# Optimization experiments

Hardware: AMD Instinct MI355X
Metric: run time of the kernel (lower is better)

Reference implementation:

```python
import jax, jax.numpy as jnp
import numpy as np

N = 25000      # nodes
E = 300000     # edges
IN = 32        # in_dim
EDF = 16       # edge_feat_dim
HID = 256      # hidden_dim (per-head dim, concat=False)
HEADS = 4
ACT = 16       # num_actions
G = 64         # graphs in batch
KW = 1024      # wire-mask query nodes


def setup_inputs() -> dict:
    key = jax.random.key(0)
    ks = jax.random.split(key, 20)
    def rn(k, shape, s=0.1):
        return jax.random.normal(k, shape, jnp.float32) * s
    return {
        "x": jax.random.normal(ks[0], (N, IN), jnp.float32),
        "edge_attr": jax.random.normal(ks[1], (E, EDF), jnp.float32),
        "wire_mask": jax.random.randint(ks[2], (KW,), 0, N, jnp.int32),
        "edge_index": jax.random.randint(ks[3], (2, E), 0, N, jnp.int32),
        "batch": jnp.sort(jax.random.randint(ks[4], (N,), 0, G, jnp.int32)),
        "enc_w1": rn(ks[5], (EDF, 32)),
        "enc_b1": jnp.zeros((32,), jnp.float32),
        "enc_w2": rn(ks[6], (32, IN * IN), 0.05),
        "enc_b2": jnp.zeros((IN * IN,), jnp.float32),
        "root_w": rn(ks[7], (IN, IN)),
        "nn_bias": jnp.zeros((IN,), jnp.float32),
        "gat1_w": rn(ks[8], (IN, HEADS * HID)),
        "gat1_asrc": rn(ks[9], (HEADS, HID)),
        "gat1_adst": rn(ks[10], (HEADS, HID)),
        "gat1_b": jnp.zeros((HID,), jnp.float32),
        "gat2_w": rn(ks[11], (HID, HEADS * HID)),
        "gat2_asrc": rn(ks[12], (HEADS, HID)),
        "gat2_adst": rn(ks[13], (HEADS, HID)),
        "gat2_b": jnp.zeros((HID,), jnp.float32),
        "wire_w": rn(ks[14], (HID, 1)),
        "wire_b": jnp.zeros((1,), jnp.float32),
        "act_w": rn(ks[15], (HID, ACT)),
        "act_b": jnp.zeros((ACT,), jnp.float32),
    }


def _gat(x, src, dst, W, a_src, a_dst, b):
    # PyG GATConv, concat=False (mean over heads), eval mode (no dropout),
    # self-loops already included in (src, dst).
    H, D = a_src.shape
    h = (x @ W).reshape(-1, H, D)                      # [N, H, D]
    es = (h * a_src[None]).sum(-1)                     # [N, H]
    ed = (h * a_dst[None]).sum(-1)                     # [N, H]
    e = jax.nn.leaky_relu(es[src] + ed[dst], negative_slope=0.2)  # [E2, H]
    m = jax.ops.segment_max(e, dst, num_segments=N)    # segment softmax (stable)
    w = jnp.exp(e - m[dst])
    den = jax.ops.segment_sum(w, dst, num_segments=N)
    alpha = w / (den[dst] + 1e-16)
    out = jax.ops.segment_sum(h[src] * alpha[..., None], dst, num_segments=N)
    return out.mean(axis=1) + b                        # [N, D]


def reference(x, edge_attr, wire_mask, edge_index, batch,
              enc_w1, enc_b1, enc_w2, enc_b2, root_w, nn_bias,
              gat1_w, gat1_asrc, gat1_adst, gat1_b,
              gat2_w, gat2_asrc, gat2_adst, gat2_b,
              wire_w, wire_b, act_w, act_b):
    src, dst = edge_index[0], edge_index[1]
    # NNConv (aggr='mean'): per-edge weight matrix from edge MLP
    We = (jax.nn.relu(edge_attr @ enc_w1 + enc_b1) @ enc_w2 + enc_b2)
    We = We.reshape(E, IN, IN)                         # [E, in, out]
    msg = jnp.einsum('ei,eio->eo', x[src], We)         # [E, out]
    s = jax.ops.segment_sum(msg, dst, num_segments=N)
    cnt = jax.ops.segment_sum(jnp.ones((E,), x.dtype), dst, num_segments=N)
    agg = s / jnp.maximum(cnt, 1.0)[:, None]
    h0 = jax.nn.relu(agg + x @ root_w + nn_bias)
    # GATConv default add_self_loops=True
    sl = jnp.arange(N, dtype=src.dtype)
    src2 = jnp.concatenate([src, sl])
    dst2 = jnp.concatenate([dst, sl])
    h1 = jax.nn.relu(_gat(h0, src2, dst2, gat1_w, gat1_asrc, gat1_adst, gat1_b))
    h2 = jax.nn.relu(_gat(h1, src2, dst2, gat2_w, gat2_asrc, gat2_adst, gat2_b))
    p_wire = (h2[wire_mask] @ wire_w + wire_b).squeeze(-1)   # [KW]
    pooled_s = jax.ops.segment_sum(h2, batch, num_segments=G)
    gc = jax.ops.segment_sum(jnp.ones((N,), h2.dtype), batch, num_segments=G)
    pooled = pooled_s / jnp.maximum(gc, 1.0)[:, None]        # global_mean_pool
    p_action = pooled @ act_w + act_b                        # [G, ACT]
    return (p_wire, p_action)
```

## Files before the change

kernel.cpp:

```cpp
#include <hip/hip_runtime.h>
#include <hip/hip_fp16.h>

#define N_NODES 25000
#define M_PAD   25024
#define N_TILES 1564
#define N_EDGES 300000
#define IN_DIM  32
#define EDFD    16
#define HIDD    256
#define HEADS   4
#define NACT    16
#define NGRAPH  64
#define KWIRE   1024
#define POOL_NB 64

typedef _Float16 half8v __attribute__((ext_vector_type(8)));
typedef __attribute__((ext_vector_type(4))) float f32x4;

__device__ __forceinline__ float leaky(float v) { return v > 0.f ? v : 0.2f * v; }

__global__ __launch_bounds__(256) void k_deg2(const int* __restrict__ ei,
                                              int* __restrict__ deg,
                                              int* __restrict__ deg2) {
    int e = blockIdx.x * 256 + threadIdx.x;
    if (e >= N_EDGES) return;
    atomicAdd(&deg[ei[N_EDGES + e]], 1);
    atomicAdd(&deg2[ei[e]], 1);
}

__global__ __launch_bounds__(256) void k_scan2(const int* __restrict__ degA, int* __restrict__ rpA,
                                               const int* __restrict__ degB, int* __restrict__ rpB) {
    const int* deg = blockIdx.x ? degB : degA;
    int* rowptr    = blockIdx.x ? rpB : rpA;
    __shared__ int part[256];
    int t = threadIdx.x;
    const int CH = 98;
    int base = t * CH;
    int s = 0;
    for (int i = 0; i < CH; ++i) {
        int idx = base + i;
        if (idx < N_NODES) s += deg[idx];
    }
    part[t] = s;
    __syncthreads();
    if (t == 0) {
        int run = 0;
        for (int i = 0; i < 256; ++i) { int v = part[i]; part[i] = run; run += v; }
    }
    __syncthreads();
    int run = part[t];
    for (int i = 0; i < CH; ++i) {
        int idx = base + i;
        if (idx < N_NODES) { rowptr[idx] = run; run += deg[idx]; }
    }
    if (N_NODES >= base && N_NODES < base + CH) rowptr[N_NODES] = run;
}

__global__ __launch_bounds__(256) void k_scatter2(const int* __restrict__ ei,
                                                  const float* __restrict__ ea,
                                                  const int* __restrict__ rowptr,
                                                  const int* __restrict__ rowptr2,
                                                  int* __restrict__ cursor,
                                                  int* __restrict__ cursor2,
                                                  int* __restrict__ csrc,
                                                  int* __restrict__ cdst,
                                                  int* __restrict__ posMap,
                                                  __half* __restrict__ eaP) {
    int e = blockIdx.x * 256 + threadIdx.x;
    if (e >= N_EDGES) return;
    int src = ei[e], dst = ei[N_EDGES + e];
    int p1 = atomicAdd(&cursor[dst], 1);
    int r1 = rowptr[dst] + p1;
    csrc[r1] = src;
    int p2 = atomicAdd(&cursor2[src], 1);
    int r2 = rowptr2[src] + p2;
    cdst[r2] = dst;
    posMap[r2] = r1;
    const float4* src4 = (const float4*)(ea + (size_t)e * EDFD);
    __half2* dp = (__half2*)(eaP + (size_t)r2 * EDFD);
    #pragma unroll
    for (int q = 0; q < EDFD / 4; ++q) {
        float4 v = src4[q];
        dp[q * 2]     = __float22half2_rn(make_float2(v.x, v.y));
        dp[q * 2 + 1] = __float22half2_rn(make_float2(v.z, v.w));
    }
}

__global__ __launch_bounds__(256) void k_prep(const float* __restrict__ w2,
                                              const float* __restrict__ W1,
                                              const float* __restrict__ W2,
                                              const float* __restrict__ a1s,
                                              const float* __restrict__ a1d,
                                              const float* __restrict__ a2s,
                                              const float* __restrict__ a2d,
                                              const float* __restrict__ x,
                                              const float* __restrict__ b2,
                                              const float* __restrict__ w1,
                                              __half* __restrict__ wtt,
                                              __half* __restrict__ wb1,
                                              __half* __restrict__ wb2,
                                              float* __restrict__ wa1,
                                              float* __restrict__ wd1,
                                              float* __restrict__ wa2,
                                              float* __restrict__ wd2,
                                              __half* __restrict__ xf,
                                              float* __restrict__ xb,
                                              __half* __restrict__ w1t) {
    int bid = blockIdx.x, t = threadIdx.x;
    if (bid < 128) {
        int idx = bid * 256 + t;
        int co = idx >> 5, i = idx & 31;
        wtt[idx] = __float2half(w2[(co >> 5) * 1024 + i * 32 + (co & 31)]);
    } else if (bid < 256) {
        int idx = (bid - 128) * 256 + t;
        int d = idx >> 7, k = idx & 127;
        int h = k >> 5, i = k & 31;
        wb1[idx] = __float2half(0.25f * W1[i * 1024 + h * 256 + d]);
    } else if (bid < 1280) {
        int idx = (bid - 256) * 256 + t;
        int d = idx >> 10, k = idx & 1023;
        int h = k >> 8, i = k & 255;
        wb2[idx] = __float2half(0.25f * W2[i * 1024 + h * 256 + d]);
    } else if (bid < 4405) {
        int idx = (bid - 1280) * 256 + t;
        if (idx >= N_NODES * 32) return;
        int n = idx >> 5, o = idx & 31;
        xf[idx] = __float2half(x[idx]);
        float s = 0.f;
        for (int i = 0; i < 32; ++i) s += x[n * 32 + i] * b2[i * 32 + o];
        xb[idx] = s;
    } else if (bid == 4405) {
        if (t >= 128) return;
        int h = t >> 5, i = t & 31;
        float s = 0.f, sd = 0.f;
        for (int d = 0; d < 256; ++d) {
            float w = W1[i * 1024 + h * 256 + d];
            s  += w * a1s[h * 256 + d];
            sd += w * a1d[h * 256 + d];
        }
        wa1[t] = s; wd1[t] = sd;
    } else if (bid < 4410) {
        int idx = (bid - 4406) * 256 + t;
        if (idx >= 1024) return;
        int h = idx >> 8, i = idx & 255;
        float s = 0.f, sd = 0.f;
        for (int d = 0; d < 256; ++d) {
            float w = W2[i * 1024 + h * 256 + d];
            s  += w * a2s[h * 256 + d];
            sd += w * a2d[h * 256 + d];
        }
        wa2[idx] = s; wd2[idx] = sd;
    } else {
        int idx = (bid - 4410) * 256 + t;
        if (idx >= 32 * EDFD) return;
        int j = idx >> 4, k = idx & 15;
        w1t[idx] = __float2half(w1[k * 32 + j]);
    }
}

__global__ __launch_bounds__(256) void k_msg3(const int* __restrict__ rowptr2,
                                              const int* __restrict__ posMap,
                                              const __half* __restrict__ eaP,
                                              const __half* __restrict__ w1t,
                                              const float* __restrict__ b1,
                                              const __half* __restrict__ T,
                                              const float* __restrict__ xb,
                                              __half* __restrict__ msgE) {
    int wv = threadIdx.x >> 6, lane = threadIdx.x & 63;
    int src = blockIdx.x * 4 + wv;
    if (src >= N_NODES) return;
    int r0 = rowptr2[src], r1 = rowptr2[src + 1];
    if (r0 == r1) return;
    int lr = lane & 15, lk = (lane >> 4) * 8;

    half8v bf0, bf1;
    const __half* Tp = T + (size_t)src * 1024;
    #pragma unroll
    for (int q = 0; q < 8; ++q) {
        bf0[q] = (_Float16)__half2float(Tp[(lk + q) * 32 + lr]);
        bf1[q] = (_Float16)__half2float(Tp[(lk + q) * 32 + 16 + lr]);
    }

    __half2 w1r[8][EDFD / 2];
    #pragma unroll
    for (int q = 0; q < 8; ++q) {
        const __half2* wp = (const __half2*)(w1t + (lk + q) * EDFD);
        #pragma unroll
        for (int k2 = 0; k2 < EDFD / 2; ++k2) w1r[q][k2] = wp[k2];
    }
    float b1r[8];
    #pragma unroll
    for (int q = 0; q < 8; ++q) b1r[q] = b1[lk + q];

    float xb0 = xb[src * 32 + lr], xb1 = xb[src * 32 + 16 + lr];
    int rbase = (lane >> 4) * 4;

    for (int t0 = r0; t0 < r1; t0 += 16) {
        int e = t0 + lr;
        bool ok = (e < r1);
        half8v afr;
        if (ok) {
            const __half2* ep = (const __half2*)(eaP + (size_t)e * EDFD);
            __half2 ea2[EDFD / 2];
            #pragma unroll
            for (int k2 = 0; k2 < EDFD / 2; ++k2) ea2[k2] = ep[k2];
            #pragma unroll
            for (int q = 0; q < 8; ++q) {
                float s = b1r[q];
                #pragma unroll
                for (int k2 = 0; k2 < EDFD / 2; ++k2) {
                    float2 v = __half22float2(ea2[k2]);
                    float2 w = __half22float2(w1r[q][k2]);
                    s += v.x * w.x + v.y * w.y;
                }
                afr[q] = (_Float16)fmaxf(s, 0.f);
            }
        } else {
            #pragma unroll
            for (int q = 0; q < 8; ++q) afr[q] = (_Float16)0.f;
        }
        f32x4 c0 = {0.f, 0.f, 0.f, 0.f}, c1 = {0.f, 0.f, 0.f, 0.f};
        c0 = __builtin_amdgcn_mfma_f32_16x16x32_f16(afr, bf0, c0, 0, 0, 0);
        c1 = __builtin_amdgcn_mfma_f32_16x16x32_f16(afr, bf1, c1, 0, 0, 0);
        #pragma unroll
        for (int r = 0; r < 4; ++r) {
            int er = t0 + rbase + r;
            if (er < r1) {
                int pm = posMap[er];
                msgE[(size_t)pm * 32 + lr]      = __float2half(c0[r] + xb0);
                msgE[(size_t)pm * 32 + 16 + lr] = __float2half(c1[r] + xb1);
            }
        }
    }
}

__global__ __launch_bounds__(256) void k_h0e(const float* __restrict__ x,
                                             const float* __restrict__ root_w,
                                             const float* __restrict__ nn_bias,
                                             const __half* __restrict__ msgE,
                                             const int* __restrict__ rowptr,
                                             const float* __restrict__ wa,
                                             const float* __restrict__ wd,
                                             __half* __restrict__ h0f,
                                             float* __restrict__ es,
                                             float* __restrict__ ed) {
    int t = threadIdx.x;
    int ng = t >> 5, o = t & 31;
    int n = blockIdx.x * 8 + ng;
    if (n >= N_NODES) return;
    float s = nn_bias[o];
    for (int k = 0; k < IN_DIM; ++k) s += x[n * IN_DIM + k] * root_w[k * 32 + o];
    int r0 = rowptr[n], r1 = rowptr[n + 1];
    float aggv = 0.f;
    for (int r = r0; r < r1; ++r)
        aggv += __half2float(msgE[(size_t)r * 32 + o]);
    float c = fmaxf((float)(r1 - r0), 1.f);
    s += aggv / c;
    float v = fmaxf(s, 0.f);
    h0f[n * IN_DIM + o] = __float2half(v);
    #pragma unroll
    for (int h = 0; h < 4; ++h) {
        float ss = v * wa[h * 32 + o];
        float dd = v * wd[h * 32 + o];
        #pragma unroll
        for (int off = 16; off; off >>= 1) {
            ss += __shfl_down(ss, off, 32);
            dd += __shfl_down(dd, off, 32);
        }
        if (o == 0) { es[n * 4 + h] = ss; ed[n * 4 + h] = dd; }
    }
}

__global__ __launch_bounds__(256, 2) void k_gemT(const __half* __restrict__ A,
                                                 const __half* __restrict__ Wt,
                                                 __half* __restrict__ C) {
    __shared__ __half cst[4][16 * 36];
    int t = threadIdx.x, wid = t >> 6, lane = t & 63;
    int lr = lane & 15, lk = (lane >> 4) * 8;

    int bid = blockIdx.x;
    int xcd = bid & 7, j = bid >> 3;
    int sx = j & 31;
    int y = ((j >> 5) << 3) | xcd;
    int n0 = sx * 32;

    half8v bfr[2];
    #pragma unroll
    for (int c = 0; c < 2; ++c)
        bfr[c] = *(const half8v*)(Wt + (size_t)(n0 + c * 16 + lr) * 32 + lk);

    int tb = (y * 4 + wid) * 4;
    for (int pp = 0; pp < 4; pp += 2) {
        int tA = tb + pp;
        if (tA >= N_TILES) break;
        int mA = tA * 16, mB = mA + 16;
        half8v aA = *(const half8v*)(A + (size_t)(mA + lr) * 32 + lk);
        half8v aB = *(const half8v*)(A + (size_t)(mB + lr) * 32 + lk);
        f32x4 acc[2][2];
        #pragma unroll
        for (int i = 0; i < 2; ++i)
            #pragma unroll
            for (int c = 0; c < 2; ++c)
                acc[i][c] = (f32x4){0.f, 0.f, 0.f, 0.f};
        acc[0][0] = __builtin_amdgcn_mfma_f32_16x16x32_f16(aA, bfr[0], acc[0][0], 0, 0, 0);
        acc[0][1] = __builtin_amdgcn_mfma_f32_16x16x32_f16(aA, bfr[1], acc[0][1], 0, 0, 0);
        acc[1][0] = __builtin_amdgcn_mfma_f32_16x16x32_f16(aB, bfr[0], acc[1][0], 0, 0, 0);
        acc[1][1] = __builtin_amdgcn_mfma_f32_16x16x32_f16(aB, bfr[1], acc[1][1], 0, 0, 0);

        int rbase = (lane >> 4) * 4;
        #pragma unroll
        for (int ti = 0; ti < 2; ++ti) {
            #pragma unroll
            for (int c = 0; c < 2; ++c)
                #pragma unroll
                for (int r = 0; r < 4; ++r)
                    cst[wid][(rbase + r) * 36 + c * 16 + lr] = __float2half(acc[ti][c][r]);
            int m0 = ti ? mB : mA;
            #pragma unroll
            for (int p = 0; p < 2; ++p) {
                int row = p * 8 + (lane >> 3), hb = lane & 7;
                float2 v = *(const float2*)((const char*)&cst[wid][0] + row * 72 + hb * 8);
                *(float2*)((char*)C + ((size_t)(m0 + row) * 1024 + n0) * 2 + hb * 8) = v;
            }
        }
    }
}

template <int K, typename OT>
__global__ __launch_bounds__(256) void k_gemmo(const __half* __restrict__ A,
                                               const __half* __restrict__ Wt,
                                               const float* __restrict__ bias,
                                               OT* __restrict__ C) {
    constexpr int CK  = 128;
    constexpr int KC  = K / CK;
    constexpr int KSC = CK / 32;
    constexpr int CB  = CK * 2;
    __shared__ __half bs[2][32 * CK];
    __shared__ float cst[4][16 * 36];
    int t = threadIdx.x, wid = t >> 6, lane = t & 63;
    int lr = lane & 15, lk = (lane >> 4) * 8;

    int bid = blockIdx.x;
    int xcd = bid & 7, rest = bid >> 3;
    int strip = rest & 7, yhi = rest >> 3;
    int y = yhi * 8 + xcd;
    if (y >= 98) return;
    int n0 = strip * 32;
    float bv0 = bias[n0 + lr], bv1 = bias[n0 + 16 + lr];
    int tb = (y * 4 + wid) * 4;
    const int swz = (lr & 7) << 4;

    f32x4 acc[2][2][2];
    #pragma unroll
    for (int pi = 0; pi < 2; ++pi)
        #pragma unroll
        for (int i = 0; i < 2; ++i)
            #pragma unroll
            for (int c = 0; c < 2; ++c)
                acc[pi][i][c] = (f32x4){0.f, 0.f, 0.f, 0.f};

    for (int i = t * 16; i < 32 * CB; i += 256 * 16) {
        int col = i / CB, offb = i % CB;
        const char* src = (const char*)Wt + ((size_t)(n0 + col) * K) * 2 + offb;
        *(float4*)((char*)bs[0] + (i ^ ((col & 7) << 4))) = *(const float4*)src;
    }
    __syncthreads();

    for (int kc = 0; kc < KC; ++kc) {
        int cur = kc & 1;
        if (kc + 1 < KC) {
            for (int i = t * 16; i < 32 * CB; i += 256 * 16) {
                int col = i / CB, offb = i % CB;
                const char* src = (const char*)Wt + (((size_t)(n0 + col) * K + (kc + 1) * CK) * 2 + offb);
                *(float4*)((char*)bs[cur ^ 1] + (i ^ ((col & 7) << 4))) = *(const float4*)src;
            }
        }
        #pragma unroll
        for (int pi = 0; pi < 2; ++pi) {
            int tA = tb + pi * 2;
            if (tA >= N_TILES) continue;
            int mA = tA * 16, mB = mA + 16;
            const __half* pA = A + (size_t)(mA + lr) * K + kc * CK + lk;
            const __half* pB = A + (size_t)(mB + lr) * K + kc * CK + lk;
            #pragma unroll
            for (int ks = 0; ks < KSC; ++ks) {
                half8v aA = *(const half8v*)(pA + (size_t)ks * 32);
                half8v aB = *(const half8v*)(pB + (size_t)ks * 32);
                half8v b0 = *(const half8v*)((const char*)bs[cur] + ((( 0 + lr) * CB + lk * 2 + ks * 64) ^ swz));
                half8v b1 = *(const half8v*)((const char*)bs[cur] + (((16 + lr) * CB + lk * 2 + ks * 64) ^ swz));
                acc[pi][0][0] = __builtin_amdgcn_mfma_f32_16x16x32_f16(aA, b0, acc[pi][0][0], 0, 0, 0);
                acc[pi][0][1] = __builtin_amdgcn_mfma_f32_16x16x32_f16(aA, b1, acc[pi][0][1], 0, 0, 0);
                acc[pi][1][0] = __builtin_amdgcn_mfma_f32_16x16x32_f16(aB, b0, acc[pi][1][0], 0, 0, 0);
                acc[pi][1][1] = __builtin_amdgcn_mfma_f32_16x16x32_f16(aB, b1, acc[pi][1][1], 0, 0, 0);
            }
        }
        if (kc + 1 < KC) __syncthreads();
    }

    int rbase = (lane >> 4) * 4;
    #pragma unroll
    for (int pi = 0; pi < 2; ++pi) {
        int tA = tb + pi * 2;
        if (tA >= N_TILES) continue;
        #pragma unroll
        for (int ti = 0; ti < 2; ++ti) {
            #pragma unroll
            for (int c = 0; c < 2; ++c)
                #pragma unroll
                for (int r = 0; r < 4; ++r)
                    cst[wid][(rbase + r) * 36 + c * 16 + lr] =
                        fmaxf(acc[pi][ti][c][r] + (c ? bv1 : bv0), 0.f);
            int m0 = tA * 16 + ti * 16;
            int row = lane >> 2, cg = lane & 3;
            const float* sp = &cst[wid][row * 36 + cg * 8];
            if constexpr (sizeof(OT) == 2) {
                __half2 o0 = __float22half2_rn(make_float2(sp[0], sp[1]));
                __half2 o1 = __float22half2_rn(make_float2(sp[2], sp[3]));
                __half2 o2 = __float22half2_rn(make_float2(sp[4], sp[5]));
                __half2 o3 = __float22half2_rn(make_float2(sp[6], sp[7]));
                float4 v = make_float4(__uint_as_float(*(unsigned*)&o0), __uint_as_float(*(unsigned*)&o1),
                                       __uint_as_float(*(unsigned*)&o2), __uint_as_float(*(unsigned*)&o3));
                *(float4*)((__half*)C + (size_t)(m0 + row) * 256 + n0 + cg * 8) = v;
            } else {
                float4 v0 = make_float4(sp[0], sp[1], sp[2], sp[3]);
                float4 v1 = make_float4(sp[4], sp[5], sp[6], sp[7]);
                float* cp = (float*)C + (size_t)(m0 + row) * 256 + n0 + cg * 8;
                *(float4*)cp = v0;
                *(float4*)(cp + 4) = v1;
            }
        }
    }
}

__global__ __launch_bounds__(256) void k_esed2(const __half* __restrict__ h1f,
                                               const float* __restrict__ wa,
                                               const float* __restrict__ wd,
                                               float* __restrict__ es,
                                               float* __restrict__ ed) {
    int n = blockIdx.x;
    int h = threadIdx.x >> 6, lane = threadIdx.x & 63;
    float s = 0.f, d2 = 0.f;
    for (int d = lane; d < 256; d += 64) {
        float v = __half2float(h1f[(size_t)n * 256 + d]);
        s  += v * wa[h * 256 + d];
        d2 += v * wd[h * 256 + d];
    }
    #pragma unroll
    for (int off = 32; off; off >>= 1) {
        s  += __shfl_down(s, off);
        d2 += __shfl_down(d2, off);
    }
    if (lane == 0) { es[n * 4 + h] = s; ed[n * 4 + h] = d2; }
}

__global__ __launch_bounds__(256) void k_agg1(const int* __restrict__ rowptr,
                                              const int* __restrict__ csrc,
                                              const float* __restrict__ es,
                                              const float* __restrict__ ed,
                                              const __half* __restrict__ h0f,
                                              __half* __restrict__ agg0) {
    int dst = blockIdx.x * 4 + (threadIdx.x >> 6);
    if (dst >= N_NODES) return;
    int lane = threadIdx.x & 63;
    int h = lane >> 4, i2 = lane & 15;
    float edv = ed[dst * 4 + h];
    float vself = leaky(es[dst * 4 + h] + edv);
    float dn = 1.f;
    int r0 = rowptr[dst], r1 = rowptr[dst + 1];

    __half2 hv = *(const __half2*)(h0f + (size_t)dst * 32 + i2 * 2);
    float2 f = __half22float2(hv);
    float ax = f.x, ay = f.y;
    for (int r = r0; r < r1; ++r) {
        int src = csrc[r];
        float w = __expf(leaky(es[src * 4 + h] + edv) - vself);
        dn += w;
        __half2 sv = *(const __half2*)(h0f + (size_t)src * 32 + i2 * 2);
        float2 g = __half22float2(sv);
        ax += w * g.x; ay += w * g.y;
    }
    float inv = 1.f / (dn + 1e-16f);
    *(__half2*)(agg0 + (size_t)dst * 128 + h * 32 + i2 * 2) =
        __float22half2_rn(make_float2(ax * inv, ay * inv));
}

__global__ __launch_bounds__(256) void k_agg2(const int* __restrict__ rowptr,
                                              const int* __restrict__ csrc,
                                              const float* __restrict__ es,
                                              const float* __restrict__ ed,
                                              const __half* __restrict__ h1f,
                                              __half* __restrict__ agg1) {
    int dst = blockIdx.x * 4 + (threadIdx.x >> 6);
    if (dst >= N_NODES) return;
    int lane = threadIdx.x & 63;
    float vs[4], edv[4], dn[4];
    float acc[4][4];
    {
        float2 q = *(const float2*)(h1f + (size_t)dst * 256 + lane * 4);
        const __half2* hq = (const __half2*)&q;
        float2 f0 = __half22float2(hq[0]), f1 = __half22float2(hq[1]);
        #pragma unroll
        for (int h = 0; h < 4; ++h) {
            edv[h] = ed[dst * 4 + h];
            vs[h] = leaky(es[dst * 4 + h] + edv[h]);
            dn[h] = 1.f;
            acc[h][0] = f0.x; acc[h][1] = f0.y;
            acc[h][2] = f1.x; acc[h][3] = f1.y;
        }
    }
    int r0 = rowptr[dst], r1 = rowptr[dst + 1];
    for (int r = r0; r < r1; ++r) {
        int src = csrc[r];
        float4 esv = *(const float4*)(es + (size_t)src * 4);
        float w0 = __expf(leaky(esv.x + edv[0]) - vs[0]);
        float w1 = __expf(leaky(esv.y + edv[1]) - vs[1]);
        float w2 = __expf(leaky(esv.z + edv[2]) - vs[2]);
        float w3 = __expf(leaky(esv.w + edv[3]) - vs[3]);
        dn[0] += w0; dn[1] += w1; dn[2] += w2; dn[3] += w3;
        float2 q = *(const float2*)(h1f + (size_t)src * 256 + lane * 4);
        const __half2* hq = (const __half2*)&q;
        float2 f0 = __half22float2(hq[0]), f1 = __half22float2(hq[1]);
        acc[0][0] += w0 * f0.x; acc[0][1] += w0 * f0.y; acc[0][2] += w0 * f1.x; acc[0][3] += w0 * f1.y;
        acc[1][0] += w1 * f0.x; acc[1][1] += w1 * f0.y; acc[1][2] += w1 * f1.x; acc[1][3] += w1 * f1.y;
        acc[2][0] += w2 * f0.x; acc[2][1] += w2 * f0.y; acc[2][2] += w2 * f1.x; acc[2][3] += w2 * f1.y;
        acc[3][0] += w3 * f0.x; acc[3][1] += w3 * f0.y; acc[3][2] += w3 * f1.x; acc[3][3] += w3 * f1.y;
    }
    #pragma unroll
    for (int h = 0; h < 4; ++h) {
        float inv = 1.f / (dn[h] + 1e-16f);
        __half2 o0 = __float22half2_rn(make_float2(acc[h][0] * inv, acc[h][1] * inv));
        __half2 o1 = __float22half2_rn(make_float2(acc[h][2] * inv, acc[h][3] * inv));
        __half2* op = (__half2*)(agg1 + (size_t)dst * 1024 + h * 256 + lane * 4);
        op[0] = o0; op[1] = o1;
    }
}

__global__ __launch_bounds__(256) void k_wirepool(const int* __restrict__ wm,
                                                  const float* __restrict__ h2,
                                                  const float* __restrict__ ww,
                                                  const float* __restrict__ wb,
                                                  const int* __restrict__ batch,
                                                  float* __restrict__ out,
                                                  float* __restrict__ pooled,
                                                  float* __restrict__ gcnt) {
    int bid = blockIdx.x;
    if (bid < KWIRE / 4) {
        int k = bid * 4 + (threadIdx.x >> 6);
        int lane = threadIdx.x & 63;
        int n = wm[k];
        float s = 0.f;
        for (int d = lane; d < 256; d += 64) s += h2[(size_t)n * 256 + d] * ww[d];
        #pragma unroll
        for (int off = 32; off; off >>= 1) s += __shfl_down(s, off);
        if (lane == 0) out[k] = s + wb[0];
        return;
    }
    int n0 = (bid - KWIRE / 4) * POOL_NB;
    int n1 = n0 + POOL_NB; if (n1 > N_NODES) n1 = N_NODES;
    int d = threadIdx.x;
    int cur = batch[n0];
    float acc = 0.f, cnt = 0.f;
    for (int n = n0; n < n1; ++n) {
        int g = batch[n];
        if (g != cur) {
            atomicAdd(&pooled[cur * 256 + d], acc);
            if (d == 0) atomicAdd(&gcnt[cur], cnt);
            acc = 0.f; cnt = 0.f; cur = g;
        }
        acc += h2[(size_t)n * 256 + d];
        cnt += 1.f;
    }
    atomicAdd(&pooled[cur * 256 + d], acc);
    if (d == 0) atomicAdd(&gcnt[cur], cnt);
}

__global__ __launch_bounds__(256) void k_act(const float* __restrict__ pooled,
                                             const float* __restrict__ gcnt,
                                             const float* __restrict__ aw,
                                             const float* __restrict__ ab,
                                             float* __restrict__ out) {
    int u = blockIdx.x * 4 + (threadIdx.x >> 6);
    int lane = threadIdx.x & 63;
    if (u >= NGRAPH * NACT) return;
    int g = u >> 4, a = u & 15;
    float c = fmaxf(gcnt[g], 1.f);
    float s = 0.f;
    for (int d = lane; d < 256; d += 64) s += pooled[g * 256 + d] * aw[d * 16 + a];
    #pragma unroll
    for (int off = 32; off; off >>= 1) s += __shfl_down(s, off);
    if (lane == 0) out[KWIRE + u] = s / c + ab[a];
}

extern "C" void kernel_launch(void* const* d_in, const int* in_sizes, int n_in,
                              void* d_out, int out_size, void* d_ws, size_t ws_size,
                              hipStream_t stream) {
    const float* x        = (const float*)d_in[0];
    const float* edge_attr= (const float*)d_in[1];
    const int*   wire_mask= (const int*)d_in[2];
    const int*   edge_idx = (const int*)d_in[3];
    const int*   batch    = (const int*)d_in[4];
    const float* enc_w1   = (const float*)d_in[5];
    const float* enc_b1   = (const float*)d_in[6];
    const float* enc_w2   = (const float*)d_in[7];
    const float* enc_b2   = (const float*)d_in[8];
    const float* root_w   = (const float*)d_in[9];
    const float* nn_bias  = (const float*)d_in[10];
    const float* gat1_w   = (const float*)d_in[11];
    const float* gat1_asrc= (const float*)d_in[12];
    const float* gat1_adst= (const float*)d_in[13];
    const float* gat1_b   = (const float*)d_in[14];
    const float* gat2_w   = (const float*)d_in[15];
    const float* gat2_asrc= (const float*)d_in[16];
    const float* gat2_adst= (const float*)d_in[17];
    const float* gat2_b   = (const float*)d_in[18];
    const float* wire_w   = (const float*)d_in[19];
    const float* wire_b   = (const float*)d_in[20];
    const float* act_w    = (const float*)d_in[21];
    const float* act_b    = (const float*)d_in[22];
    float* out = (float*)d_out;

    float* ws = (float*)d_ws;
    size_t off = 0;
    __half* T16   = (__half*)(ws + off); off += (size_t)M_PAD * 1024 / 2;
    __half* agg1f = (__half*)(ws + off); off += (size_t)M_PAD * 1024 / 2;
    __half* agg0f = (__half*)(ws + off); off += (size_t)M_PAD * 128 / 2;
    __half* h0f   = (__half*)(ws + off); off += (size_t)M_PAD * 32 / 2;
    __half* h1f   = (__half*)(ws + off); off += (size_t)M_PAD * 256 / 2;
    __half* xf    = (__half*)(ws + off); off += (size_t)M_PAD * 32 / 2;
    __half* eaP   = (__half*)(ws + off); off += (size_t)N_EDGES * EDFD / 2;
    __half* msgE  = (__half*)(ws + off); off += (size_t)N_EDGES * 32 / 2;
    float* xb     = ws + off; off += 800000;
    float* esb    = ws + off; off += 100000;
    float* edb    = ws + off; off += 100000;
    float* h2     = ws + off; off += (size_t)M_PAD * 256;
    float* pooled = ws + off; off += NGRAPH * 256;
    float* gcnt   = ws + off; off += NGRAPH;
    int* deg      = (int*)(ws + off); off += 25600;
    int* deg2     = (int*)(ws + off); off += 25600;
    int* cursor   = (int*)(ws + off); off += 25600;
    int* cursor2  = (int*)(ws + off); off += 25600;
    int* rowptr   = (int*)(ws + off); off += 25600;
    int* rowptr2  = (int*)(ws + off); off += 25600;
    int* csrc     = (int*)(ws + off); off += N_EDGES;
    int* cdst     = (int*)(ws + off); off += N_EDGES;
    int* posMap   = (int*)(ws + off); off += N_EDGES;
    __half* wtt   = (__half*)(ws + off); off += 16384;
    __half* wb1t  = (__half*)(ws + off); off += 16384;
    __half* wb2t  = (__half*)(ws + off); off += 131072;
    __half* w1t   = (__half*)(ws + off); off += 256;
    float* wa1    = ws + off; off += 128;
    float* wd1    = ws + off; off += 128;
    float* wa2    = ws + off; off += 1024;
    float* wd2    = ws + off; off += 1024;

    const int GBT = 3328;
    const int GBO = 832;

    hipMemsetAsync(deg, 0, 4 * 25600 * sizeof(int), stream);
    k_deg2<<<(N_EDGES + 255) / 256, 256, 0, stream>>>(edge_idx, deg, deg2);
    k_scan2<<<2, 256, 0, stream>>>(deg, rowptr, deg2, rowptr2);
    k_scatter2<<<(N_EDGES + 255) / 256, 256, 0, stream>>>(edge_idx, edge_attr, rowptr, rowptr2,
                                                          cursor, cursor2, csrc, cdst, posMap, eaP);

    k_prep<<<4412, 256, 0, stream>>>(enc_w2, gat1_w, gat2_w, gat1_asrc, gat1_adst,
                                     gat2_asrc, gat2_adst, x, enc_b2, enc_w1,
                                     wtt, wb1t, wb2t, wa1, wd1, wa2, wd2, xf, xb, w1t);

    k_gemT<<<GBT, 256, 0, stream>>>(xf, wtt, T16);
    k_msg3<<<(N_NODES + 3) / 4, 256, 0, stream>>>(rowptr2, posMap, eaP,
                                                  w1t, enc_b1, T16, xb, msgE);
    k_h0e<<<(N_NODES + 7) / 8, 256, 0, stream>>>(x, root_w, nn_bias, msgE, rowptr,
                                                 wa1, wd1, h0f, esb, edb);

    k_agg1<<<(N_NODES + 3) / 4, 256, 0, stream>>>(rowptr, csrc, esb, edb, h0f, agg0f);
    k_gemmo<128, __half><<<GBO, 256, 0, stream>>>(agg0f, wb1t, gat1_b, h1f);
    k_esed2<<<N_NODES, 256, 0, stream>>>(h1f, wa2, wd2, esb, edb);

    k_agg2<<<(N_NODES + 3) / 4, 256, 0, stream>>>(rowptr, csrc, esb, edb, h1f, agg1f);
    k_gemmo<1024, float><<<GBO, 256, 0, stream>>>(agg1f, wb2t, gat2_b, h2);

    hipMemsetAsync(pooled, 0, (NGRAPH * 256 + NGRAPH) * sizeof(float), stream);
    k_wirepool<<<KWIRE / 4 + (N_NODES + POOL_NB - 1) / POOL_NB, 256, 0, stream>>>(
        wire_mask, h2, wire_w, wire_b, batch, out, pooled, gcnt);
    k_act<<<NGRAPH * NACT / 4, 256, 0, stream>>>(pooled, gcnt, act_w, act_b, out);
}
```

Baseline: 430.3 us.

## Halve per-wave tile count in output GEMM and double grid for occupancy

The output GEMM kernel now gives each wave two 16-row tiles instead of four, so the grid grows from 832 to 1600 blocks and accumulator registers are halved. Launch bounds now request 4 blocks per CU. A loads for each k-chunk are hoisted into register arrays before the MFMA loop so that memory latency overlaps with compute. In exchange, each weight strip staged in shared memory is reused across fewer rows, which roughly doubles global reads of the weights.

```diff
diff --git a/kernel.cpp b/kernel.cpp
--- a/kernel.cpp
+++ b/kernel.cpp
@@ -327,10 +327,10 @@
 }
 
 template <int K, typename OT>
-__global__ __launch_bounds__(256) void k_gemmo(const __half* __restrict__ A,
-                                               const __half* __restrict__ Wt,
-                                               const float* __restrict__ bias,
-                                               OT* __restrict__ C) {
+__global__ __launch_bounds__(256, 4) void k_gemmo(const __half* __restrict__ A,
+                                                  const __half* __restrict__ Wt,
+                                                  const float* __restrict__ bias,
+                                                  OT* __restrict__ C) {
     constexpr int CK  = 128;
     constexpr int KC  = K / CK;
     constexpr int KSC = CK / 32;
@@ -344,20 +344,20 @@
     int xcd = bid & 7, rest = bid >> 3;
     int strip = rest & 7, yhi = rest >> 3;
     int y = yhi * 8 + xcd;
-    if (y >= 98) return;
+    if (y >= 196) return;
     int n0 = strip * 32;
     float bv0 = bias[n0 + lr], bv1 = bias[n0 + 16 + lr];
-    int tb = (y * 4 + wid) * 4;
+    int tb = y * 8 + wid * 2;
+    int tA0 = tb     < N_TILES ? tb     : N_TILES - 1;
+    int tA1 = tb + 1 < N_TILES ? tb + 1 : N_TILES - 1;
     const int swz = (lr & 7) << 4;
 
-    f32x4 acc[2][2][2];
-    #pragma unroll
-    for (int pi = 0; pi < 2; ++pi)
-        #pragma unroll
-        for (int i = 0; i < 2; ++i)
-            #pragma unroll
-            for (int c = 0; c < 2; ++c)
-                acc[pi][i][c] = (f32x4){0.f, 0.f, 0.f, 0.f};
+    f32x4 acc[2][2];
+    #pragma unroll
+    for (int i = 0; i < 2; ++i)
+        #pragma unroll
+        for (int c = 0; c < 2; ++c)
+            acc[i][c] = (f32x4){0.f, 0.f, 0.f, 0.f};
 
     for (int i = t * 16; i < 32 * CB; i += 256 * 16) {
         int col = i / CB, offb = i % CB;
@@ -365,6 +365,9 @@
         *(float4*)((char*)bs[0] + (i ^ ((col & 7) << 4))) = *(const float4*)src;
     }
     __syncthreads();
+
+    const __half* pA0 = A + (size_t)(tA0 * 16 + lr) * K + lk;
+    const __half* pA1 = A + (size_t)(tA1 * 16 + lr) * K + lk;
 
     for (int kc = 0; kc < KC; ++kc) {
         int cur = kc & 1;
@@ -375,59 +378,51 @@
                 *(float4*)((char*)bs[cur ^ 1] + (i ^ ((col & 7) << 4))) = *(const float4*)src;
             }
         }
-        #pragma unroll
-        for (int pi = 0; pi < 2; ++pi) {
-            int tA = tb + pi * 2;
-            if (tA >= N_TILES) continue;
-            int mA = tA * 16, mB = mA + 16;
-            const __half* pA = A + (size_t)(mA + lr) * K + kc * CK + lk;
-            const __half* pB = A + (size_t)(mB + lr) * K + kc * CK + lk;
+        half8v aH0[KSC], aH1[KSC];
+        #pragma unroll
+        for (int ks = 0; ks < KSC; ++ks) {
+            aH0[ks] = *(const half8v*)(pA0 + kc * CK + ks * 32);
+            aH1[ks] = *(const half8v*)(pA1 + kc * CK + ks * 32);
+        }
+        #pragma unroll
+        for (int ks = 0; ks < KSC; ++ks) {
+            half8v b0 = *(const half8v*)((const char*)bs[cur] + ((( 0 + lr) * CB + lk * 2 + ks * 64) ^ swz));
+            half8v b1 = *(const half8v*)((const char*)bs[cur] + (((16 + lr) * CB + lk * 2 + ks * 64) ^ swz));
+            acc[0][0] = __builtin_amdgcn_mfma_f32_16x16x32_f16(aH0[ks], b0, acc[0][0], 0, 0, 0);
+            acc[0][1] = __builtin_amdgcn_mfma_f32_16x16x32_f16(aH0[ks], b1, acc[0][1], 0, 0, 0);
+            acc[1][0] = __builtin_amdgcn_mfma_f32_16x16x32_f16(aH1[ks], b0, acc[1][0], 0, 0, 0);
+            acc[1][1] = __builtin_amdgcn_mfma_f32_16x16x32_f16(aH1[ks], b1, acc[1][1], 0, 0, 0);
+        }
+        if (kc + 1 < KC) __syncthreads();
+    }
+
+    int rbase = (lane >> 4) * 4;
+    #pragma unroll
+    for (int ti = 0; ti < 2; ++ti) {
+        if (tb + ti >= N_TILES) break;
+        #pragma unroll
+        for (int c = 0; c < 2; ++c)
             #pragma unroll
-            for (int ks = 0; ks < KSC; ++ks) {
-                half8v aA = *(const half8v*)(pA + (size_t)ks * 32);
-                half8v aB = *(const half8v*)(pB + (size_t)ks * 32);
-                half8v b0 = *(const half8v*)((const char*)bs[cur] + ((( 0 + lr) * CB + lk * 2 + ks * 64) ^ swz));
-                half8v b1 = *(const half8v*)((const char*)bs[cur] + (((16 + lr) * CB + lk * 2 + ks * 64) ^ swz));
-                acc[pi][0][0] = __builtin_amdgcn_mfma_f32_16x16x32_f16(aA, b0, acc[pi][0][0], 0, 0, 0);
-                acc[pi][0][1] = __builtin_amdgcn_mfma_f32_16x16x32_f16(aA, b1, acc[pi][0][1], 0, 0, 0);
-                acc[pi][1][0] = __builtin_amdgcn_mfma_f32_16x16x32_f16(aB, b0, acc[pi][1][0], 0, 0, 0);
-                acc[pi][1][1] = __builtin_amdgcn_mfma_f32_16x16x32_f16(aB, b1, acc[pi][1][1], 0, 0, 0);
-            }
-        }
-        if (kc + 1 < KC) __syncthreads();
-    }
-
-    int rbase = (lane >> 4) * 4;
-    #pragma unroll
-    for (int pi = 0; pi < 2; ++pi) {
-        int tA = tb + pi * 2;
-        if (tA >= N_TILES) continue;
-        #pragma unroll
-        for (int ti = 0; ti < 2; ++ti) {
-            #pragma unroll
-            for (int c = 0; c < 2; ++c)
-                #pragma unroll
-                for (int r = 0; r < 4; ++r)
-                    cst[wid][(rbase + r) * 36 + c * 16 + lr] =
-                        fmaxf(acc[pi][ti][c][r] + (c ? bv1 : bv0), 0.f);
-            int m0 = tA * 16 + ti * 16;
-            int row = lane >> 2, cg = lane & 3;
-            const float* sp = &cst[wid][row * 36 + cg * 8];
-            if constexpr (sizeof(OT) == 2) {
-                __half2 o0 = __float22half2_rn(make_float2(sp[0], sp[1]));
-                __half2 o1 = __float22half2_rn(make_float2(sp[2], sp[3]));
-                __half2 o2 = __float22half2_rn(make_float2(sp[4], sp[5]));
-                __half2 o3 = __float22half2_rn(make_float2(sp[6], sp[7]));
-                float4 v = make_float4(__uint_as_float(*(unsigned*)&o0), __uint_as_float(*(unsigned*)&o1),
-                                       __uint_as_float(*(unsigned*)&o2), __uint_as_float(*(unsigned*)&o3));
-                *(float4*)((__half*)C + (size_t)(m0 + row) * 256 + n0 + cg * 8) = v;
-            } else {
-                float4 v0 = make_float4(sp[0], sp[1], sp[2], sp[3]);
-                float4 v1 = make_float4(sp[4], sp[5], sp[6], sp[7]);
-                float* cp = (float*)C + (size_t)(m0 + row) * 256 + n0 + cg * 8;
-                *(float4*)cp = v0;
-                *(float4*)(cp + 4) = v1;
-            }
+            for (int r = 0; r < 4; ++r)
+                cst[wid][(rbase + r) * 36 + c * 16 + lr] =
+                    fmaxf(acc[ti][c][r] + (c ? bv1 : bv0), 0.f);
+        int m0 = (tb + ti) * 16;
+        int row = lane >> 2, cg = lane & 3;
+        const float* sp = &cst[wid][row * 36 + cg * 8];
+        if constexpr (sizeof(OT) == 2) {
+            __half2 o0 = __float22half2_rn(make_float2(sp[0], sp[1]));
+            __half2 o1 = __float22half2_rn(make_float2(sp[2], sp[3]));
+            __half2 o2 = __float22half2_rn(make_float2(sp[4], sp[5]));
+            __half2 o3 = __float22half2_rn(make_float2(sp[6], sp[7]));
+            float4 v = make_float4(__uint_as_float(*(unsigned*)&o0), __uint_as_float(*(unsigned*)&o1),
+                                   __uint_as_float(*(unsigned*)&o2), __uint_as_float(*(unsigned*)&o3));
+            *(float4*)((__half*)C + (size_t)(m0 + row) * 256 + n0 + cg * 8) = v;
+        } else {
+            float4 v0 = make_float4(sp[0], sp[1], sp[2], sp[3]);
+            float4 v1 = make_float4(sp[4], sp[5], sp[6], sp[7]);
+            float* cp = (float*)C + (size_t)(m0 + row) * 256 + n0 + cg * 8;
+            *(float4*)cp = v0;
+            *(float4*)(cp + 4) = v1;
         }
     }
 }
@@ -654,7 +649,7 @@
     float* wd2    = ws + off; off += 1024;
 
     const int GBT = 3328;
-    const int GBO = 832;
+    const int GBO = 1600;
 
     hipMemsetAsync(deg, 0, 4 * 25600 * sizeof(int), stream);
     k_deg2<<<(N_EDGES + 255) / 256, 256, 0, stream>>>(edge_idx, deg, deg2);
```

New measurement: 426.7 us. Within noise of the previous version (-0.8%).
